# Optimization experiments

Measured on AMD Instinct MI355X. Metric: run time of the kernel, lower is better.

Reference implementation:

```python
import jax, jax.numpy as jnp
import numpy as np

DIM = 70      # voxel grid side
NE = 6        # element channels
B = 8         # batch
TARGET = 29   # TARGET_NUM in source


def _xavier(key, shape, fan_in, fan_out):
    lim = float(np.sqrt(6.0 / (fan_in + fan_out)))
    return jax.random.uniform(key, shape, jnp.float32, -lim, lim)


def setup_inputs() -> dict:
    key = jax.random.key(0)
    ks = jax.random.split(key, 12)
    # Sparse binary occupancy grid: ~34 atoms per channel per molecule.
    x = (jax.random.uniform(ks[0], (B, NE, DIM, DIM, DIM)) < 1e-4).astype(jnp.float32)
    sigma = 2.0 * jnp.ones((NE,), jnp.float32)
    k3 = 3 * 3 * 3
    conv1_w = _xavier(ks[1], (32, NE, 3, 3, 3), NE * k3, 32 * k3)
    conv2_w = _xavier(ks[2], (64, 32, 3, 3, 3), 32 * k3, 64 * k3)
    conv3_w = _xavier(ks[3], (128, 64, 3, 3, 3), 64 * k3, 128 * k3)
    conv4_w = _xavier(ks[4], (256, 128, 3, 3, 3), 128 * k3, 256 * k3)
    conv1_b = jnp.full((32,), 0.01, jnp.float32)
    conv2_b = jnp.full((64,), 0.01, jnp.float32)
    conv3_b = jnp.full((128,), 0.01, jnp.float32)
    conv4_b = jnp.full((256,), 0.01, jnp.float32)
    fc1_w = _xavier(ks[5], (1024, 2048), 2048, 1024)
    fc1_b = jnp.full((1024,), 0.01, jnp.float32)
    fc2_w = _xavier(ks[6], (TARGET, 1024), 1024, TARGET)
    fc2_b = jax.random.uniform(ks[7], (TARGET,), jnp.float32, -1.0 / 32.0, 1.0 / 32.0)
    return dict(x=x, sigma=sigma,
                conv1_w=conv1_w, conv1_b=conv1_b, conv2_w=conv2_w, conv2_b=conv2_b,
                conv3_w=conv3_w, conv3_b=conv3_b, conv4_w=conv4_w, conv4_b=conv4_b,
                fc1_w=fc1_w, fc1_b=fc1_b, fc2_w=fc2_w, fc2_b=fc2_b)


def _blur(x, sigma):
    # Faithful to source: Gaussian centered at raw voxel INDICES (x0,y0,z0 from
    # nonzero()) but evaluated on SHIFTED coords arange(-dim/2, dim/2).
    # Separable Gaussian -> three 1D contractions instead of per-atom loops.
    coords = jnp.arange(DIM, dtype=jnp.float32) - DIM / 2.0   # -35 .. 34
    idx = jnp.arange(DIM, dtype=jnp.float32)                   # 0 .. 69
    d2 = (coords[:, None] - idx[None, :]) ** 2                 # [70,70]
    G = jnp.exp(-d2[None, :, :] / (2.0 * sigma[:, None, None] ** 2))  # [e,out,in]
    mask = (x != 0).astype(x.dtype)                            # [b,e,i,j,k]
    t = jnp.einsum('beijk,eai->beajk', mask, G)
    t = jnp.einsum('beajk,epj->beapk', t, G)
    cube = jnp.einsum('beapk,eqk->beapq', t, G)                # [b,e,70,70,70]
    return cube


def _conv3d(h, w, b):
    y = jax.lax.conv_general_dilated(h, w, (1, 1, 1), 'VALID',
                                     dimension_numbers=('NCDHW', 'OIDHW', 'NCDHW'))
    return y + b[None, :, None, None, None]


def _pool(h):
    return jax.lax.reduce_window(h, -jnp.inf, jax.lax.max,
                                 (1, 1, 2, 2, 2), (1, 1, 2, 2, 2), 'VALID')


def reference(x, sigma, conv1_w, conv1_b, conv2_w, conv2_b, conv3_w, conv3_b,
              conv4_w, conv4_b, fc1_w, fc1_b, fc2_w, fc2_b):
    h = _blur(x, sigma)
    h = jax.nn.relu(_pool(_conv3d(h, conv1_w, conv1_b)))
    h = jax.nn.relu(_pool(_conv3d(h, conv2_w, conv2_b)))
    h = jax.nn.relu(_pool(_conv3d(h, conv3_w, conv3_b)))
    h = jax.nn.relu(_pool(_conv3d(h, conv4_w, conv4_b)))  # [B,256,2,2,2]
    v = h.reshape(x.shape[0], -1)                          # [B,2048]
    y1 = jax.nn.relu(v @ fc1_w.T + fc1_b)
    y2 = y1 @ fc2_w.T + fc2_b                              # [B,29]
    return y2
```

## Files before the change

kernel.cpp:

```cpp
#include <hip/hip_runtime.h>
#include <hip/hip_bf16.h>

#define DIMV 70
#define NEL 6
#define BATCH 8

typedef unsigned short u16;
typedef unsigned int u32;
typedef __bf16 bf16x8 __attribute__((ext_vector_type(8)));
typedef short short8v __attribute__((ext_vector_type(8)));
typedef float f32x4 __attribute__((ext_vector_type(4)));

__device__ __forceinline__ u16 f2bf(float f) {
  __hip_bfloat16 h = __float2bfloat16(f);
  return __builtin_bit_cast(u16, h);
}
__device__ __forceinline__ float bf2f(u16 u) {
  unsigned int x = ((unsigned int)u) << 16;
  return __builtin_bit_cast(float, x);
}

__global__ __launch_bounds__(256) void k_scan(const float* __restrict__ x,
                                              int* __restrict__ cnt,
                                              int* __restrict__ lists) {
  const int N4 = (BATCH * NEL * DIMV * DIMV * DIMV) / 4;
  int i = blockIdx.x * 256 + threadIdx.x;
  if (i >= N4) return;
  float4 v = ((const float4*)x)[i];
  int ch = i / 85750;
  int local = 4 * i - ch * 343000;
  float f[4] = {v.x, v.y, v.z, v.w};
#pragma unroll
  for (int k = 0; k < 4; ++k) {
    if (f[k] != 0.f) {
      int slot = atomicAdd(&cnt[ch], 1);
      if (slot < 512) lists[ch * 512 + slot] = local + k;
    }
  }
}

__global__ __launch_bounds__(256) void k_gather(const int* __restrict__ cnt,
                                                const int* __restrict__ lists,
                                                const float* __restrict__ sigma,
                                                u32* __restrict__ cube, int b0) {
  const int z = blockIdx.x;
  const int bl = blockIdx.y / NEL;
  const int e = blockIdx.y % NEL;
  const int chG = (b0 + bl) * NEL + e;
  const int tid = threadIdx.x;
  float sg = sigma[e];
  float inv2s2 = 1.f / (2.f * sg * sg);

  __shared__ int s_n;
  __shared__ int s_idx[512];
  __shared__ float s_wz[512];
  __shared__ float s_wy[32 * 70];
  __shared__ float s_wx[32 * 70];

  if (tid == 0) s_n = 0;
  __syncthreads();
  int n = min(cnt[chG], 512);
  for (int t = tid; t < n; t += 256) {
    int idx = lists[chG * 512 + t];
    int i0 = idx / 4900;
    float d = (float)(z - 35 - i0);
    float wz = expf(-d * d * inv2s2);
    if (wz > 1e-30f) {
      int s = atomicAdd(&s_n, 1);
      s_idx[s] = idx;
      s_wz[s] = wz;
    }
  }
  __syncthreads();
  int m = s_n;

  float acc[20];
#pragma unroll
  for (int k = 0; k < 20; ++k) acc[k] = 0.f;

  for (int t0 = 0; t0 < m; t0 += 32) {
    int tn = min(32, m - t0);
    __syncthreads();
    for (int u = tid; u < tn * 70; u += 256) {
      int t = u / 70, pos = u % 70;
      int idx = s_idx[t0 + t];
      int j0 = (idx / 70) % 70, k0 = idx % 70;
      float dy = (float)(pos - 35 - j0);
      float dx = (float)(pos - 35 - k0);
      s_wy[t * 70 + pos] = s_wz[t0 + t] * expf(-dy * dy * inv2s2);
      s_wx[t * 70 + pos] = expf(-dx * dx * inv2s2);
    }
    __syncthreads();
#pragma unroll
    for (int k = 0; k < 20; ++k) {
      int v = tid + k * 256;
      if (v < 4900) {
        int y = v / 70, xx = v % 70;
        float a = 0.f;
        for (int t = 0; t < tn; ++t)
          a = fmaf(s_wy[t * 70 + y], s_wx[t * 70 + xx], a);
        acc[k] += a;
      }
    }
  }
  size_t base = ((size_t)(bl * NEL + e) * DIMV + z) * 4900;
#pragma unroll
  for (int k = 0; k < 20; ++k) {
    int v = tid + k * 256;
    if (v < 4900) {
      float val = acc[k];
      u16 hi = f2bf(val);
      u16 lo = f2bf(val - bf2f(hi));
      cube[base + v] = ((u32)hi << 16) | (u32)lo;
    }
  }
}

__device__ __forceinline__ void pack_s_one(const float* __restrict__ w,
                                           u16* __restrict__ A, int CINL,
                                           int idx) {
  int K2 = CINL * 81;
  int o = idx / K2, k = idx % K2;
  int kb = k >> 5, r = k & 31;
  int g = r >> 3, e = r & 7;
  int kk = kb % 27;
  int t = kb / 27;
  int snum = CINL >> 5;
  int sub = t % snum, s = t / snum;
  int c = sub * 32 + 8 * g + e;
  float wv = w[(o * CINL + c) * 27 + kk];
  u16 hi = f2bf(wv);
  A[idx] = (s == 2) ? f2bf(wv - bf2f(hi)) : hi;
}

__global__ __launch_bounds__(256) void k_packall(
    const float* __restrict__ w1, u16* __restrict__ Ah, u16* __restrict__ Al,
    const float* __restrict__ w2, u16* __restrict__ ap2,
    const float* __restrict__ w3, u16* __restrict__ ap3,
    const float* __restrict__ w4, u16* __restrict__ ap4,
    int* __restrict__ cnt) {
  const int R0 = 48;
  const int R1 = 32 * 224;
  const int R2 = 64 * 2592;
  const int R3 = 128 * 5184;
  const int R4 = 256 * 10368;
  int gi = blockIdx.x * 256 + threadIdx.x;
  if (gi < R0) {
    cnt[gi] = 0;
    return;
  }
  gi -= R0;
  if (gi < R1) {
    int o = gi / 224, k = gi % 224;
    int kk = k >> 5, r = k & 31;
    int g = r >> 3, e = r & 7;
    int off = 4 * kk + g;
    u16 h = 0, l = 0;
    if (off < 27 && e < 6) {
      float wv = w1[(o * 6 + e) * 27 + off];
      u16 hi = f2bf(wv);
      h = hi;
      l = f2bf(wv - bf2f(hi));
    }
    Ah[gi] = h;
    Al[gi] = l;
    return;
  }
  gi -= R1;
  if (gi < R2) { pack_s_one(w2, ap2, 32, gi); return; }
  gi -= R2;
  if (gi < R3) { pack_s_one(w3, ap3, 64, gi); return; }
  gi -= R3;
  if (gi < R4) { pack_s_one(w4, ap4, 128, gi); return; }
}

__global__ __launch_bounds__(256) void k_conv1(
    const u16* __restrict__ Ah, const u16* __restrict__ Al,
    const u32* __restrict__ cube, const float* __restrict__ bias,
    float* __restrict__ out, int b0) {
  __shared__ __align__(16) u16 Thi[1120 * 8];
  __shared__ __align__(16) u16 Tlo[1120 * 8];
  const int tid = threadIdx.x;
  const int wave = tid >> 6, lane = tid & 63;
  const int n = lane & 15, g = lane >> 4;
  const int py = blockIdx.x % 34, pz = blockIdx.x / 34;
  const int blb = blockIdx.y, bG = blb + b0;

  u32* thw = (u32*)Thi;
  u32* tlw = (u32*)Tlo;
  for (int i = tid; i < 4480; i += 256) {
    int j = i & 3, pos = i >> 2;
    int xx = pos % 70, line = pos / 70;
    int z = 2 * pz + (line >> 2), y = 2 * py + (line & 3);
    u32 a = 0, b2 = 0;
    if (j < 3) {
      size_t p0 = (((size_t)(blb * 6 + 2 * j) * 70 + z) * 70 + y) * 70 + xx;
      a = cube[p0];
      b2 = cube[p0 + 343000];
    }
    thw[pos * 4 + j] = (a >> 16) | (b2 & 0xFFFF0000u);
    tlw[pos * 4 + j] = (a & 0xFFFFu) | (b2 << 16);
  }
  __syncthreads();

  const int rc = wave;
  f32x4 acc[2][5] = {};
  for (int kk = 0; kk < 7; ++kk) {
    bf16x8 a0[2], a2[2];
#pragma unroll
    for (int mt = 0; mt < 2; ++mt) {
      a0[mt] = __builtin_bit_cast(
          bf16x8, *(const short8v*)(Ah + (size_t)(mt * 16 + n) * 224 + kk * 32 + 8 * g));
      a2[mt] = __builtin_bit_cast(
          bf16x8, *(const short8v*)(Al + (size_t)(mt * 16 + n) * 224 + kk * 32 + 8 * g));
    }
    int off = min(4 * kk + g, 26);
    int dz = off / 9, dy = (off / 3) % 3, dx = off % 3;
    int line = ((rc >> 1) + dz) * 4 + (rc & 1) + dy;
    __builtin_amdgcn_s_setprio(1);
#pragma unroll
    for (int nt = 0; nt < 5; ++nt) {
      int x_in = nt * 16 + n + dx;
      if (x_in > 69) x_in = 69;
      int cell = (line * 70 + x_in) * 8;
      bf16x8 bh = __builtin_bit_cast(bf16x8, *(const short8v*)&Thi[cell]);
      bf16x8 bl = __builtin_bit_cast(bf16x8, *(const short8v*)&Tlo[cell]);
#pragma unroll
      for (int mt = 0; mt < 2; ++mt) {
        acc[mt][nt] = __builtin_amdgcn_mfma_f32_16x16x32_bf16(a0[mt], bh, acc[mt][nt], 0, 0, 0);
        acc[mt][nt] = __builtin_amdgcn_mfma_f32_16x16x32_bf16(a2[mt], bh, acc[mt][nt], 0, 0, 0);
        acc[mt][nt] = __builtin_amdgcn_mfma_f32_16x16x32_bf16(a0[mt], bl, acc[mt][nt], 0, 0, 0);
      }
    }
    __builtin_amdgcn_s_setprio(0);
  }
  __syncthreads();
  float* Pb = (float*)Thi;
#pragma unroll
  for (int mt = 0; mt < 2; ++mt) {
#pragma unroll
    for (int nt = 0; nt < 5; ++nt) {
#pragma unroll
      for (int r = 0; r < 4; ++r) {
        float v = acc[mt][nt][r];
        float v2 = fmaxf(v, __shfl_xor(v, 1));
        int o = mt * 16 + 4 * g + r;
        int px = (nt * 16 + n) >> 1;
        if (!(n & 1) && px < 34) Pb[(wave * 32 + o) * 34 + px] = v2;
      }
    }
  }
  __syncthreads();
  for (int t = tid; t < 1088; t += 256) {
    int o = t / 34, px = t % 34;
    float m = fmaxf(fmaxf(Pb[t], Pb[1088 + t]), fmaxf(Pb[2176 + t], Pb[3264 + t]));
    float rv = fmaxf(m + bias[o], 0.f);
    out[((((size_t)bG * 32 + o) * 34 + pz) * 34 + py) * 34 + px] = rv;
  }
}

template <int CINL, int COUT, int DIN, int WAVES, int XS>
__global__ __launch_bounds__(WAVES * 64) void k_conv_m(
    const u16* __restrict__ Apack, const float* __restrict__ in,
    const float* __restrict__ bias, float* __restrict__ out) {
  constexpr int DP = (DIN - 2) / 2;
  constexpr int DPL = DP / XS;
  constexpr int XLOC = (XS > 1) ? (DPL * 2 + 2) : DIN;
  constexpr int SNUM = CINL / 32;
  constexpr int K2 = 81 * CINL;
  __shared__ __align__(16) u16 Thi[16 * XLOC * 32];
  __shared__ __align__(16) u16 Tlo[16 * XLOC * 32];

  const int tid = threadIdx.x;
  const int wave = tid >> 6, lane = tid & 63;
  const int n = lane & 15, g = lane >> 4;
  const int xh = blockIdx.x % XS;
  const int tb = blockIdx.x / XS;
  const int py = tb % DP, pz = tb / DP;
  const int b = blockIdx.y;

  f32x4 acc[4][1] = {};

  for (int sub = 0; sub < SNUM; ++sub) {
    if (sub) __syncthreads();
    const int E2 = 16 * XLOC * 16;
    for (int i = tid; i < E2; i += WAVES * 64) {
      int xl = i % XLOC;
      int t2 = i / XLOC;
      int jp = t2 & 15;
      int line = t2 >> 4;
      int z = 2 * pz + (line >> 2), y = 2 * py + (line & 3);
      int xx = xh * (DPL * 2) + xl;
      int c = sub * 32 + 2 * jp;
      size_t base = (((size_t)(b * CINL + c) * DIN + z) * DIN + y) * DIN + xx;
      float v0 = in[base];
      float v1 = in[base + (size_t)DIN * DIN * DIN];
      u16 h0 = f2bf(v0), h1 = f2bf(v1);
      u16 l0 = f2bf(v0 - bf2f(h0));
      u16 l1 = f2bf(v1 - bf2f(h1));
      int byte = (line * XLOC + xl) * 64 + (((jp >> 2) ^ ((xl >> 1) & 3)) << 4) + ((jp & 3) << 2);
      *(u32*)((char*)Thi + byte) = (u32)h0 | ((u32)h1 << 16);
      *(u32*)((char*)Tlo + byte) = (u32)l0 | ((u32)l1 << 16);
    }
    __syncthreads();
    for (int kk = 0; kk < 27; ++kk) {
      const u16* abase = Apack + (size_t)(wave * 16 + n) * K2 + 8 * g;
      bf16x8 a0 = __builtin_bit_cast(
          bf16x8, *(const short8v*)(abase + ((0 * SNUM + sub) * 27 + kk) * 32));
      bf16x8 a2 = __builtin_bit_cast(
          bf16x8, *(const short8v*)(abase + ((2 * SNUM + sub) * 27 + kk) * 32));
      int dz = kk / 9, dy = (kk / 3) % 3, dx = kk % 3;
      __builtin_amdgcn_s_setprio(1);
#pragma unroll
      for (int rc = 0; rc < 4; ++rc) {
        int line = ((rc >> 1) + dz) * 4 + (rc & 1) + dy;
        int xl = n + dx;
        if (xl > XLOC - 1) xl = XLOC - 1;
        int byte = (line * XLOC + xl) * 64 + ((g ^ ((xl >> 1) & 3)) << 4);
        bf16x8 bh = __builtin_bit_cast(bf16x8, *(const short8v*)((const char*)Thi + byte));
        bf16x8 bl = __builtin_bit_cast(bf16x8, *(const short8v*)((const char*)Tlo + byte));
        acc[rc][0] = __builtin_amdgcn_mfma_f32_16x16x32_bf16(a0, bh, acc[rc][0], 0, 0, 0);
        acc[rc][0] = __builtin_amdgcn_mfma_f32_16x16x32_bf16(a2, bh, acc[rc][0], 0, 0, 0);
        acc[rc][0] = __builtin_amdgcn_mfma_f32_16x16x32_bf16(a0, bl, acc[rc][0], 0, 0, 0);
      }
      __builtin_amdgcn_s_setprio(0);
    }
  }
#pragma unroll
  for (int r = 0; r < 4; ++r) {
    float v = fmaxf(fmaxf(acc[0][0][r], acc[1][0][r]),
                    fmaxf(acc[2][0][r], acc[3][0][r]));
    float v2 = fmaxf(v, __shfl_xor(v, 1));
    int o = wave * 16 + 4 * g + r;
    int pxl = n >> 1;
    if (!(n & 1) && pxl < DPL) {
      int px = xh * DPL + pxl;
      float rv = fmaxf(v2 + bias[o], 0.f);
      out[((((size_t)b * COUT + o) * DP + pz) * DP + py) * DP + px] = rv;
    }
  }
}

__global__ __launch_bounds__(512) void k_conv4ks(
    const u16* __restrict__ Apack, const float* __restrict__ in,
    float* __restrict__ P) {
  __shared__ __align__(16) u16 T[343 * 32];
  const int tid = threadIdx.x;
  const int wave = tid >> 6, lane = tid & 63;
  const int n = lane & 15, g = lane >> 4;
  const int q = blockIdx.x;
  const int third = q >> 3;
  const int r8 = q & 7;
  const int ph = r8 >> 2, sub = r8 & 3;
  const int b = blockIdx.y;

  for (int i = tid; i < 343 * 16; i += 512) {
    int jp = i & 15, pos = i >> 4;
    int c = sub * 32 + 2 * jp;
    const float* src = in + (size_t)(b * 128 + c) * 343 + pos;
    float v0 = src[0];
    float v1 = src[343];
    u16 h0 = f2bf(v0), h1 = f2bf(v1);
    u16 a0 = ph ? f2bf(v0 - bf2f(h0)) : h0;
    u16 a1 = ph ? f2bf(v1 - bf2f(h1)) : h1;
    int byte = pos * 64 + (((jp >> 2) ^ (pos & 3)) << 4) + ((jp & 3) << 2);
    *(u32*)((char*)T + byte) = (u32)a0 | ((u32)a1 << 16);
  }
  __syncthreads();

  f32x4 acc[2][4] = {};
  const int ys = n >> 2, xo = n & 3;
  for (int t = 0; t < 9; ++t) {
    int kk = third * 9 + t;
    int dz = kk / 9, dy = (kk / 3) % 3, dx = kk % 3;
    bf16x8 a0[2], a2[2];
#pragma unroll
    for (int mr = 0; mr < 2; ++mr) {
      int mtile = wave + 8 * mr;
      const u16* base = Apack + (size_t)(mtile * 16 + n) * 10368 + 8 * g;
      if (ph == 0) {
        a0[mr] = __builtin_bit_cast(
            bf16x8, *(const short8v*)(base + ((0 * 4 + sub) * 27 + kk) * 32));
        a2[mr] = __builtin_bit_cast(
            bf16x8, *(const short8v*)(base + ((2 * 4 + sub) * 27 + kk) * 32));
      } else {
        a0[mr] = __builtin_bit_cast(
            bf16x8, *(const short8v*)(base + ((1 * 4 + sub) * 27 + kk) * 32));
      }
    }
    int ybase = (ys + dy) * 7 + xo + dx;
#pragma unroll
    for (int zr = 0; zr < 4; ++zr) {
      int pos = (zr + dz) * 49 + ybase;
      int byte = pos * 64 + ((g ^ (pos & 3)) << 4);
      bf16x8 bfr = __builtin_bit_cast(bf16x8, *(const short8v*)((const char*)T + byte));
#pragma unroll
      for (int mr = 0; mr < 2; ++mr) {
        acc[mr][zr] = __builtin_amdgcn_mfma_f32_16x16x32_bf16(a0[mr], bfr, acc[mr][zr], 0, 0, 0);
        if (ph == 0)
          acc[mr][zr] = __builtin_amdgcn_mfma_f32_16x16x32_bf16(a2[mr], bfr, acc[mr][zr], 0, 0, 0);
      }
    }
  }
  float* Pq = P + (size_t)(q * 8 + b) * 16384;
#pragma unroll
  for (int mr = 0; mr < 2; ++mr) {
    int mtile = wave + 8 * mr;
#pragma unroll
    for (int zr = 0; zr < 4; ++zr) {
#pragma unroll
      for (int r = 0; r < 4; ++r) {
        int o = mtile * 16 + 4 * g + r;
        Pq[o * 64 + zr * 16 + n] = acc[mr][zr][r];
      }
    }
  }
}

__global__ __launch_bounds__(256) void k_fin4(const float* __restrict__ P,
                                              const float* __restrict__ bias,
                                              float* __restrict__ h4) {
  int t = blockIdx.x * 256 + threadIdx.x;
  if (t >= 16384) return;
  int w = t & 7;
  int o = (t >> 3) & 255;
  int b = t >> 11;
  int pd = w >> 2, p2 = (w >> 1) & 1, pw = w & 1;
  float m = -1e30f;
#pragma unroll
  for (int dz = 0; dz < 2; ++dz)
#pragma unroll
    for (int dy = 0; dy < 2; ++dy)
#pragma unroll
      for (int dx = 0; dx < 2; ++dx) {
        int pos = (2 * pd + dz) * 16 + (2 * p2 + dy) * 4 + (2 * pw + dx);
        float s = 0.f;
        for (int q = 0; q < 24; ++q)
          s += P[(size_t)(q * 8 + b) * 16384 + o * 64 + pos];
        m = fmaxf(m, s);
      }
  h4[(size_t)b * 2048 + o * 8 + w] = fmaxf(m + bias[o], 0.f);
}

__global__ __launch_bounds__(256) void k_fc1(const float* __restrict__ v,
                                             const float* __restrict__ W,
                                             const float* __restrict__ bias,
                                             float* __restrict__ y) {
  int o = blockIdx.x;
  int tid = threadIdx.x;
  int wave = tid >> 6, lane = tid & 63;
  __shared__ float red[4][8];
  float acc[8] = {};
  const float* wp = W + (size_t)o * 2048 + wave * 512;
  const float* vp = v + wave * 512;
  for (int k = lane; k < 512; k += 64) {
    float wv = wp[k];
#pragma unroll
    for (int bb = 0; bb < 8; ++bb)
      acc[bb] = fmaf(vp[bb * 2048 + k], wv, acc[bb]);
  }
#pragma unroll
  for (int off = 32; off; off >>= 1)
#pragma unroll
    for (int bb = 0; bb < 8; ++bb) acc[bb] += __shfl_xor(acc[bb], off);
  if (lane == 0) {
#pragma unroll
    for (int bb = 0; bb < 8; ++bb) red[wave][bb] = acc[bb];
  }
  __syncthreads();
  if (tid < 8) {
    float s = red[0][tid] + red[1][tid] + red[2][tid] + red[3][tid];
    y[tid * 1024 + o] = fmaxf(s + bias[o], 0.f);
  }
}

__global__ __launch_bounds__(64) void k_fc2(const float* __restrict__ v,
                                            const float* __restrict__ W,
                                            const float* __restrict__ bias,
                                            float* __restrict__ y) {
  int o = blockIdx.x;
  int lane = threadIdx.x;
  float acc[8] = {};
  for (int k = lane; k < 1024; k += 64) {
    float wv = W[o * 1024 + k];
#pragma unroll
    for (int bb = 0; bb < 8; ++bb)
      acc[bb] = fmaf(v[bb * 1024 + k], wv, acc[bb]);
  }
#pragma unroll
  for (int off = 32; off; off >>= 1)
#pragma unroll
    for (int bb = 0; bb < 8; ++bb) acc[bb] += __shfl_xor(acc[bb], off);
  if (lane == 0) {
    float bo = bias[o];
#pragma unroll
    for (int bb = 0; bb < 8; ++bb) y[bb * 29 + o] = acc[bb] + bo;
  }
}

extern "C" void kernel_launch(void* const* d_in, const int* in_sizes, int n_in,
                              void* d_out, int out_size, void* d_ws, size_t ws_size,
                              hipStream_t stream) {
  const float* x   = (const float*)d_in[0];
  const float* sig = (const float*)d_in[1];
  const float* w1  = (const float*)d_in[2];
  const float* b1  = (const float*)d_in[3];
  const float* w2  = (const float*)d_in[4];
  const float* b2  = (const float*)d_in[5];
  const float* w3  = (const float*)d_in[6];
  const float* b3  = (const float*)d_in[7];
  const float* w4  = (const float*)d_in[8];
  const float* b4  = (const float*)d_in[9];
  const float* fw1 = (const float*)d_in[10];
  const float* fb1 = (const float*)d_in[11];
  const float* fw2 = (const float*)d_in[12];
  const float* fb2 = (const float*)d_in[13];

  char* ws = (char*)d_ws;
  u32*   cube4 = (u32*)(ws + 0);
  float* P     = (float*)(ws + 0);
  float* h1    = (float*)(ws + 32928000);
  u16*   ah1   = (u16*)(ws + 73200000);
  u16*   al1   = (u16*)(ws + 73250000);
  u16*   ap2   = (u16*)(ws + 73300000);
  u16*   ap3   = (u16*)(ws + 73700000);
  u16*   ap4   = (u16*)(ws + 75100000);
  float* h2    = (float*)(ws + 80500000);
  float* h3    = (float*)(ws + 89000000);
  float* h4    = (float*)(ws + 90500000);
  float* y1    = (float*)(ws + 90600000);
  int*   cnt   = (int*)(ws + 90700000);
  int*   lists = (int*)(ws + 90701024);

  const int PACK_TOTAL = 48 + 32 * 224 + 64 * 2592 + 128 * 5184 + 256 * 10368;
  k_packall<<<(PACK_TOTAL + 255) / 256, 256, 0, stream>>>(
      w1, ah1, al1, w2, ap2, w3, ap3, w4, ap4, cnt);

  const int N4 = (BATCH * NEL * DIMV * DIMV * DIMV) / 4;
  k_scan<<<(N4 + 255) / 256, 256, 0, stream>>>(x, cnt, lists);

  for (int half = 0; half < 2; ++half) {
    int b0 = 4 * half;
    k_gather<<<dim3(DIMV, 4 * NEL), 256, 0, stream>>>(cnt, lists, sig, cube4, b0);
    k_conv1<<<dim3(34 * 34, 4), 256, 0, stream>>>(ah1, al1, cube4, b1, h1, b0);
  }

  k_conv_m<32,  64, 34, 4, 2><<<dim3(16 * 16 * 2, 8), 256, 0, stream>>>(ap2, h1, b2, h2);
  k_conv_m<64, 128, 16, 8, 1><<<dim3(7 * 7, 8),       512, 0, stream>>>(ap3, h2, b3, h3);

  k_conv4ks<<<dim3(24, 8), 512, 0, stream>>>(ap4, h3, P);
  k_fin4<<<64, 256, 0, stream>>>(P, b4, h4);

  k_fc1<<<1024, 256, 0, stream>>>(h4, fw1, fb1, y1);
  k_fc2<<<29, 64, 0, stream>>>(y1, fw2, fb2, (float*)d_out);
}
```

Measured before the change: 480.9 us.

## Add dedicated conv2 kernel using 32x32x16 MFMA with split-bf16 packing

Replaces the generic templated conv2 kernel with a specialized k_conv2y that uses 32x32x16 bf16 MFMA tiles and a register accumulator of 16 floats per lane. The weight packing for conv2 is changed to a new layout (hi/lo split per 16-channel chunk) matching the new kernel's A-fragment loads, and the input tile is staged in LDS with an XOR swizzle. The aim is fewer MFMA instructions and better fragment reuse for the 3-term split-bf16 emulation of fp32. Risk is in the different accumulator row mapping and pooling indexing, plus A fragments being read straight from global memory each iteration.

```diff
diff --git a/kernel.cpp b/kernel.cpp
--- a/kernel.cpp
+++ b/kernel.cpp
@@ -10,6 +10,7 @@
 typedef __bf16 bf16x8 __attribute__((ext_vector_type(8)));
 typedef short short8v __attribute__((ext_vector_type(8)));
 typedef float f32x4 __attribute__((ext_vector_type(4)));
+typedef float f32x16 __attribute__((ext_vector_type(16)));
 
 __device__ __forceinline__ u16 f2bf(float f) {
   __hip_bfloat16 h = __float2bfloat16(f);
@@ -167,7 +168,17 @@
     return;
   }
   gi -= R1;
-  if (gi < R2) { pack_s_one(w2, ap2, 32, gi); return; }
+  if (gi < R2) {
+    int o = gi / 2592, k = gi % 2592;
+    int chunk = k >> 4, kc = k & 15;
+    int s = chunk / 54, r2 = chunk % 54;
+    int ch = r2 / 27, kk2 = r2 % 27;
+    int c = ch * 16 + kc;
+    float wv = w2[(o * 32 + c) * 27 + kk2];
+    u16 hi = f2bf(wv);
+    ap2[gi] = (s == 2) ? f2bf(wv - bf2f(hi)) : hi;
+    return;
+  }
   gi -= R2;
   if (gi < R3) { pack_s_one(w3, ap3, 64, gi); return; }
   gi -= R3;
@@ -256,6 +267,91 @@
     float m = fmaxf(fmaxf(Pb[t], Pb[1088 + t]), fmaxf(Pb[2176 + t], Pb[3264 + t]));
     float rv = fmaxf(m + bias[o], 0.f);
     out[((((size_t)bG * 32 + o) * 34 + pz) * 34 + py) * 34 + px] = rv;
+  }
+}
+
+__global__ __launch_bounds__(256) void k_conv2y(
+    const u16* __restrict__ Apack, const float* __restrict__ in,
+    const float* __restrict__ bias, float* __restrict__ out) {
+  constexpr int DIN = 34, DP = 16, DPL = 8, XLOC = 18, COUT = 64, CINL = 32;
+  __shared__ __align__(16) u16 Thi[16 * XLOC * 32];
+  __shared__ __align__(16) u16 Tlo[16 * XLOC * 32];
+
+  const int tid = threadIdx.x;
+  const int wave = tid >> 6, lane = tid & 63;
+  const int p = lane & 31, gk = lane >> 5;
+  const int m = wave >> 1, rcp = wave & 1;
+  const int x = p & 15;
+  const int rc = 2 * rcp + (p >> 4);
+  const int xh = blockIdx.x & 1;
+  const int tb = blockIdx.x >> 1;
+  const int py = tb % DP, pz = tb / DP;
+  const int b = blockIdx.y;
+
+  f32x16 acc = {};
+
+  const int E2 = 16 * XLOC * 16;
+  for (int i = tid; i < E2; i += 256) {
+    int xl = i % XLOC;
+    int t2 = i / XLOC;
+    int jp = t2 & 15;
+    int line = t2 >> 4;
+    int z = 2 * pz + (line >> 2), y = 2 * py + (line & 3);
+    int xx = xh * 16 + xl;
+    int c = 2 * jp;
+    size_t base = (((size_t)(b * CINL + c) * DIN + z) * DIN + y) * DIN + xx;
+    float v0 = in[base];
+    float v1 = in[base + (size_t)DIN * DIN * DIN];
+    u16 h0 = f2bf(v0), h1 = f2bf(v1);
+    u16 l0 = f2bf(v0 - bf2f(h0));
+    u16 l1 = f2bf(v1 - bf2f(h1));
+    int byte = (line * XLOC + xl) * 64 + (((jp >> 2) ^ ((xl >> 1) & 3)) << 4) + ((jp & 3) << 2);
+    *(u32*)((char*)Thi + byte) = (u32)h0 | ((u32)h1 << 16);
+    *(u32*)((char*)Tlo + byte) = (u32)l0 | ((u32)l1 << 16);
+  }
+  __syncthreads();
+
+  for (int kk = 0; kk < 27; ++kk) {
+    int dz = kk / 9, dy = (kk / 3) % 3, dx = kk % 3;
+    int line = ((rc >> 1) + dz) * 4 + (rc & 1) + dy;
+    int xl = x + dx;
+    __builtin_amdgcn_s_setprio(1);
+#pragma unroll
+    for (int ch = 0; ch < 2; ++ch) {
+      const u16* abase = Apack + (size_t)(m * 32 + p) * 2592 + 8 * gk;
+      bf16x8 a0 = __builtin_bit_cast(
+          bf16x8, *(const short8v*)(abase + ((0 * 2 + ch) * 27 + kk) * 16));
+      bf16x8 a2 = __builtin_bit_cast(
+          bf16x8, *(const short8v*)(abase + ((2 * 2 + ch) * 27 + kk) * 16));
+      int slot = (ch * 2 + gk) ^ ((xl >> 1) & 3);
+      int byte = (line * XLOC + xl) * 64 + slot * 16;
+      bf16x8 bh = __builtin_bit_cast(bf16x8, *(const short8v*)((const char*)Thi + byte));
+      bf16x8 bl = __builtin_bit_cast(bf16x8, *(const short8v*)((const char*)Tlo + byte));
+      acc = __builtin_amdgcn_mfma_f32_32x32x16_bf16(a0, bh, acc, 0, 0, 0);
+      acc = __builtin_amdgcn_mfma_f32_32x32x16_bf16(a2, bh, acc, 0, 0, 0);
+      acc = __builtin_amdgcn_mfma_f32_32x32x16_bf16(a0, bl, acc, 0, 0, 0);
+    }
+    __builtin_amdgcn_s_setprio(0);
+  }
+  __syncthreads();
+  float* Pb = (float*)Thi;
+#pragma unroll
+  for (int r = 0; r < 16; ++r) {
+    float v = acc[r];
+    float v2 = fmaxf(v, __shfl_xor(v, 1));
+    int mrow = (r & 3) + 8 * (r >> 2) + 4 * gk;
+    int o = m * 32 + mrow;
+    int pxl = x >> 1;
+    if (!(x & 1)) Pb[(rc * COUT + o) * DPL + pxl] = v2;
+  }
+  __syncthreads();
+  for (int t = tid; t < COUT * DPL; t += 256) {
+    int o = t / DPL, pxl = t % DPL;
+    float mx = fmaxf(fmaxf(Pb[t], Pb[COUT * DPL + t]),
+                     fmaxf(Pb[2 * COUT * DPL + t], Pb[3 * COUT * DPL + t]));
+    float rv = fmaxf(mx + bias[o], 0.f);
+    int px = xh * DPL + pxl;
+    out[((((size_t)b * COUT + o) * DP + pz) * DP + py) * DP + px] = rv;
   }
 }
 
@@ -545,8 +641,8 @@
     k_conv1<<<dim3(34 * 34, 4), 256, 0, stream>>>(ah1, al1, cube4, b1, h1, b0);
   }
 
-  k_conv_m<32,  64, 34, 4, 2><<<dim3(16 * 16 * 2, 8), 256, 0, stream>>>(ap2, h1, b2, h2);
-  k_conv_m<64, 128, 16, 8, 1><<<dim3(7 * 7, 8),       512, 0, stream>>>(ap3, h2, b3, h3);
+  k_conv2y<<<dim3(16 * 16 * 2, 8), 256, 0, stream>>>(ap2, h1, b2, h2);
+  k_conv_m<64, 128, 16, 8, 1><<<dim3(7 * 7, 8), 512, 0, stream>>>(ap3, h2, b3, h3);
 
   k_conv4ks<<<dim3(24, 8), 512, 0, stream>>>(ap4, h3, P);
   k_fin4<<<64, 256, 0, stream>>>(P, b4, h4);
```

Result: slower. 579.6 us (+20.5%).
